# Optimization experiments

Hardware: AMD Instinct MI355X
Metric: run time of the kernel (lower is better)

Reference implementation:

```python
import jax, jax.numpy as jnp
import numpy as np

NEG_SLOPE = 0.01  # torch nn.LeakyReLU default


def setup_inputs() -> dict:
    key = jax.random.key(0)
    k1, k2, k3, k4, k5 = jax.random.split(key, 5)
    N, K, S, H = 50000, 32, 128, 4
    x = jax.random.normal(k1, (N, S), dtype=jnp.float32)          # node sentence vectors
    neighbors = jax.random.randint(k2, (N, K), 0, N)              # padded neighbor ids
    mask = jax.random.uniform(k3, (N, K)) < 0.75                  # valid-neighbor mask
    # DQA.B_ij per head: Linear(2*S -> 1), init std=0.05
    W = jax.random.normal(k4, (H, 2 * S), dtype=jnp.float32) * 0.05
    b = jax.random.normal(k5, (H,), dtype=jnp.float32) * 0.05
    return {"x": x, "W": W, "b": b, "neighbors": neighbors,
            "mask": mask, "propagate_count": 2}


def _leaky_relu(v):
    return jnp.where(v >= 0, v, NEG_SLOPE * v)


def reference(x, W, b, neighbors, mask, propagate_count):
    # x: [N,S]; W: [H,2S]; b: [H]; neighbors: [N,K] int; mask: [N,K] bool
    S = x.shape[-1]
    wa, wb = W[:, :S], W[:, S:]  # score = wa.x_center + wb.x_row + b

    def step(h):
        sa = h @ wa.T                                  # [N,H] center contribution
        sb = h @ wb.T                                  # [N,H] row contribution
        s_self = _leaky_relu(sa + sb + b)              # [N,H]   row 0 (self)
        s_nbr = _leaky_relu(sa[:, None, :] + sb[neighbors] + b)  # [N,K,H]
        s_nbr = jnp.where(mask[:, :, None], s_nbr, -jnp.inf)
        s_all = jnp.concatenate([s_self[:, None, :], s_nbr], axis=1)  # [N,K+1,H]
        p = jax.nn.softmax(s_all, axis=1)              # softmax over rows
        xg = h[neighbors]                              # [N,K,S] gather
        # weighted sum of rows, per head
        out = p[:, 0, :, None] * h[:, None, :] \
              + jnp.einsum('nkh,nks->nhs', p[:, 1:, :], xg)  # [N,H,S]
        # D_attention: sum over heads / n_heads, then ReLU
        return jax.nn.relu(out.mean(axis=1))           # [N,S]

    for _ in range(int(propagate_count)):
        x = step(x)
    return x
```

## Files before the change

### kernel.cpp

```cpp
#include <hip/hip_runtime.h>
#include <math.h>

#define S_DIM   128
#define K_NB    32
#define H_HEADS 4
#define WL_STRIDE 288
#define NSLOT   36

#if defined(__has_builtin)
#  if __has_builtin(__builtin_amdgcn_permlane16_swap)
#    define HAVE_PL16 1
#  endif
#  if __has_builtin(__builtin_amdgcn_permlane32_swap)
#    define HAVE_PL32 1
#  endif
#endif

__device__ __forceinline__ float lrelu(float v) { return fmaxf(v, 0.01f * v); }

__device__ __forceinline__ float bfly_add16(float x) {
#ifdef HAVE_PL16
    auto r = __builtin_amdgcn_permlane16_swap(__float_as_uint(x), __float_as_uint(x), false, false);
    return __uint_as_float(r[0]) + __uint_as_float(r[1]);
#else
    return x + __shfl_xor(x, 16, 64);
#endif
}
__device__ __forceinline__ float bfly_add32(float x) {
#ifdef HAVE_PL32
    auto r = __builtin_amdgcn_permlane32_swap(__float_as_uint(x), __float_as_uint(x), false, false);
    return __uint_as_float(r[0]) + __uint_as_float(r[1]);
#else
    return x + __shfl_xor(x, 32, 64);
#endif
}

__device__ __forceinline__ unsigned bf16rne(float f) {
    unsigned u = __float_as_uint(f);
    return (u + 0x7fffu + ((u >> 16) & 1u)) >> 16;
}
__device__ __forceinline__ unsigned pack2(float lo, float hi) {
    return bf16rne(lo) | (bf16rne(hi) << 16);
}

__global__ __launch_bounds__(256) void proj_kernel(const float* __restrict__ h,
                                                   const float* __restrict__ W,
                                                   float* __restrict__ sasb,
                                                   unsigned* __restrict__ hb_out,
                                                   const unsigned int* __restrict__ maskw,
                                                   int* __restrict__ flag, int N) {
    __shared__ float Wl[H_HEADS * 2 * S_DIM];
    for (int i = threadIdx.x; i < 1024; i += 256) Wl[i] = W[i];

    if (blockIdx.x == 0) {
        __shared__ int nb, nf;
        if (threadIdx.x == 0) { nb = 0; nf = 0; }
        __syncthreads();
        bool bin = true, f32 = true;
        for (int i = threadIdx.x; i < 2048; i += 256) {
            unsigned v = maskw[i];
            if (v > 1u) bin = false;
            if (v != 0u && v != 0x3F800000u) f32 = false;
        }
        if (!bin) atomicOr(&nb, 1);
        if (!f32) atomicOr(&nf, 1);
        __syncthreads();
        if (threadIdx.x == 0) *flag = nb ? (nf ? 2 : 1) : 0;
    }
    __syncthreads();

    const int wv = threadIdx.x >> 6;
    const int lane = threadIdx.x & 63;
    const int n = blockIdx.x * 4 + wv;
    if (n >= N) return;

    const float2 hv = reinterpret_cast<const float2*>(h)[(size_t)n * 64 + lane];
    hb_out[(size_t)n * 64 + lane] = pack2(hv.x, hv.y);

    const int c = 2 * lane;
    float p0 = hv.x * Wl[0 * 256 + c] + hv.y * Wl[0 * 256 + c + 1];
    float p1 = hv.x * Wl[1 * 256 + c] + hv.y * Wl[1 * 256 + c + 1];
    float p2 = hv.x * Wl[2 * 256 + c] + hv.y * Wl[2 * 256 + c + 1];
    float p3 = hv.x * Wl[3 * 256 + c] + hv.y * Wl[3 * 256 + c + 1];
    float p4 = hv.x * Wl[0 * 256 + 128 + c] + hv.y * Wl[0 * 256 + 128 + c + 1];
    float p5 = hv.x * Wl[1 * 256 + 128 + c] + hv.y * Wl[1 * 256 + 128 + c + 1];
    float p6 = hv.x * Wl[2 * 256 + 128 + c] + hv.y * Wl[2 * 256 + 128 + c + 1];
    float p7 = hv.x * Wl[3 * 256 + 128 + c] + hv.y * Wl[3 * 256 + 128 + c + 1];

    const float a0 = p0 + __shfl_xor(p0, 32, 64);
    const float a1 = p1 + __shfl_xor(p1, 32, 64);
    const float a2 = p2 + __shfl_xor(p2, 32, 64);
    const float a3 = p3 + __shfl_xor(p3, 32, 64);
    const float a4 = p4 + __shfl_xor(p4, 32, 64);
    const float a5 = p5 + __shfl_xor(p5, 32, 64);
    const float a6 = p6 + __shfl_xor(p6, 32, 64);
    const float a7 = p7 + __shfl_xor(p7, 32, 64);
    const bool lo = lane < 32;
    float r0 = lo ? a0 : a4, r1 = lo ? a1 : a5, r2 = lo ? a2 : a6, r3 = lo ? a3 : a7;
#pragma unroll
    for (int off = 16; off; off >>= 1) {
        r0 += __shfl_xor(r0, off, 64);
        r1 += __shfl_xor(r1, off, 64);
        r2 += __shfl_xor(r2, off, 64);
        r3 += __shfl_xor(r3, off, 64);
    }
    if (lane == 0)
        *reinterpret_cast<float4*>(sasb + (size_t)n * 8) = make_float4(r0, r1, r2, r3);
    if (lane == 32)
        *reinterpret_cast<float4*>(sasb + (size_t)n * 8 + 4) = make_float4(r0, r1, r2, r3);
}

__global__ __launch_bounds__(256) void attn_kernel(const uint4* __restrict__ hb,
                                                   const float* __restrict__ sasb,
                                                   const float* __restrict__ bvec,
                                                   const int* __restrict__ nbr,
                                                   const void* __restrict__ mask,
                                                   const int* __restrict__ maskmode,
                                                   float* __restrict__ fout,
                                                   uint4* __restrict__ hb_out,
                                                   float* __restrict__ sasb_next,
                                                   const float* __restrict__ W, int N) {
    __shared__ float2 qr_sh[4][NSLOT];
    __shared__ float Wl[H_HEADS * WL_STRIDE];

    if (sasb_next) {
        for (int i = threadIdx.x; i < 1024; i += 256) {
            const int hh = i >> 8, c = i & 255;
            Wl[hh * WL_STRIDE + c + (c >> 3)] = W[i];
        }
        __syncthreads();
    }

    const int wv = threadIdx.x >> 6;
    const int lane = threadIdx.x & 63;
    const int n = blockIdx.x * 4 + wv;
    if (n >= N) return;
    const int mode = *maskmode;

    const float b0 = bvec[0], b1 = bvec[1], b2 = bvec[2], b3 = bvec[3];
    const float4 sa = *reinterpret_cast<const float4*>(sasb + (size_t)n * 8);
    const float4 sbs = *reinterpret_cast<const float4*>(sasb + (size_t)n * 8 + 4);
    const float es0 = __expf(lrelu(sa.x + sbs.x + b0));
    const float es1 = __expf(lrelu(sa.y + sbs.y + b1));
    const float es2 = __expf(lrelu(sa.z + sbs.z + b2));
    const float es3 = __expf(lrelu(sa.w + sbs.w + b3));

    float l0 = -INFINITY, l1 = -INFINITY, l2 = -INFINITY, l3 = -INFINITY;
    int row = 0;
    bool valid = false;
    if (lane < K_NB) {
        row = nbr[(size_t)n * K_NB + lane];
        if (mode == 0)
            valid = reinterpret_cast<const int*>(mask)[(size_t)n * K_NB + lane] != 0;
        else if (mode == 1)
            valid = reinterpret_cast<const float*>(mask)[(size_t)n * K_NB + lane] != 0.f;
        else
            valid = reinterpret_cast<const unsigned char*>(mask)[(size_t)n * K_NB + lane] != 0;
    }
    if (valid) {
        const float4 sbr = *reinterpret_cast<const float4*>(sasb + (size_t)row * 8 + 4);
        l0 = lrelu(sa.x + sbr.x + b0);
        l1 = lrelu(sa.y + sbr.y + b1);
        l2 = lrelu(sa.z + sbr.z + b2);
        l3 = lrelu(sa.w + sbr.w + b3);
    }

    const float e0 = __expf(l0);
    const float e1 = __expf(l1);
    const float e2 = __expf(l2);
    const float e3 = __expf(l3);

    float s0 = bfly_add16(e0), s1 = bfly_add16(e1);
    float s2 = bfly_add16(e2), s3 = bfly_add16(e3);
#pragma unroll
    for (int off = 8; off; off >>= 1) {
        s0 += __shfl_xor(s0, off, 64);
        s1 += __shfl_xor(s1, off, 64);
        s2 += __shfl_xor(s2, off, 64);
        s3 += __shfl_xor(s3, off, 64);
    }
    s0 += es0; s1 += es1; s2 += es2; s3 += es3;
    const float i0 = __builtin_amdgcn_rcpf(s0);
    const float i1 = __builtin_amdgcn_rcpf(s1);
    const float i2 = __builtin_amdgcn_rcpf(s2);
    const float i3 = __builtin_amdgcn_rcpf(s3);

    const unsigned long long bm = __ballot(valid);
    const int nv1 = __popcll(bm) + 1;
    {
        const int ps = nv1 + lane;
        if (ps < NSLOT) qr_sh[wv][ps] = make_float2(0.f, __int_as_float(n));
    }
    if (valid) {
        const int pos = 1 + __popcll(bm & ((1ull << lane) - 1ull));
        qr_sh[wv][pos] = make_float2(
            0.25f * (e0 * i0 + e1 * i1 + e2 * i2 + e3 * i3), __int_as_float(row));
    }
    if (lane == 0)
        qr_sh[wv][0] = make_float2(
            0.25f * (es0 * i0 + es1 * i1 + es2 * i2 + es3 * i3), __int_as_float(n));

    const int grp = lane >> 4;
    const int sl = lane & 15;

    float2 qr[9];
#pragma unroll
    for (int t = 0; t < 9; ++t) qr[t] = qr_sh[wv][grp + 4 * t];

    uint4 v[9];
#pragma unroll
    for (int t = 0; t < 9; ++t) {
        const unsigned idx = ((unsigned)__float_as_int(qr[t].y) << 4) + (unsigned)sl;
        v[t] = hb[idx];
    }

    float acc[8];
#pragma unroll
    for (int j = 0; j < 8; ++j) acc[j] = 0.f;
#pragma unroll
    for (int t = 0; t < 9; ++t) {
        const float q = qr[t].x;
        acc[0] += q * __uint_as_float(v[t].x << 16);
        acc[1] += q * __uint_as_float(v[t].x & 0xffff0000u);
        acc[2] += q * __uint_as_float(v[t].y << 16);
        acc[3] += q * __uint_as_float(v[t].y & 0xffff0000u);
        acc[4] += q * __uint_as_float(v[t].z << 16);
        acc[5] += q * __uint_as_float(v[t].z & 0xffff0000u);
        acc[6] += q * __uint_as_float(v[t].w << 16);
        acc[7] += q * __uint_as_float(v[t].w & 0xffff0000u);
    }

#pragma unroll
    for (int j = 0; j < 8; ++j) {
        acc[j] = bfly_add16(acc[j]);
        acc[j] = bfly_add32(acc[j]);
        acc[j] = fmaxf(acc[j], 0.f);
    }

    if (lane < 32) {
        const int g1 = grp & 1;
        const float a0 = g1 ? acc[4] : acc[0];
        const float a1 = g1 ? acc[5] : acc[1];
        const float a2 = g1 ? acc[6] : acc[2];
        const float a3 = g1 ? acc[7] : acc[3];
        if (hb_out) {
            uint2 o;
            o.x = pack2(a0, a1);
            o.y = pack2(a2, a3);
            reinterpret_cast<uint2*>(hb_out)[(size_t)n * 32 + sl * 2 + g1] = o;
        }
        if (fout) {
            reinterpret_cast<float4*>(fout)[(size_t)n * 32 + sl * 2 + g1] =
                make_float4(a0, a1, a2, a3);
        }
    }

    if (sasb_next) {
        const int base = (lane >> 5) ? 128 : 0;
        const int boff = base + (base >> 3) + sl * 9;
        float r0 = 0.f, r1 = 0.f, r2 = 0.f, r3 = 0.f;
#pragma unroll
        for (int j = 0; j < 8; ++j) {
            const float a = acc[j];
            r0 += a * Wl[0 * WL_STRIDE + boff + j];
            r1 += a * Wl[1 * WL_STRIDE + boff + j];
            r2 += a * Wl[2 * WL_STRIDE + boff + j];
            r3 += a * Wl[3 * WL_STRIDE + boff + j];
        }
#pragma unroll
        for (int off = 8; off; off >>= 1) {
            r0 += __shfl_xor(r0, off, 64);
            r1 += __shfl_xor(r1, off, 64);
            r2 += __shfl_xor(r2, off, 64);
            r3 += __shfl_xor(r3, off, 64);
        }
        if (lane == 0)
            *reinterpret_cast<float4*>(sasb_next + (size_t)n * 8) = make_float4(r0, r1, r2, r3);
        if (lane == 32)
            *reinterpret_cast<float4*>(sasb_next + (size_t)n * 8 + 4) = make_float4(r0, r1, r2, r3);
    }
}


extern "C" void kernel_launch(void* const* d_in, const int* in_sizes, int n_in,
                              void* d_out, int out_size, void* d_ws, size_t ws_size,
                              hipStream_t stream) {
    const float* x = (const float*)d_in[0];
    const float* W = (const float*)d_in[1];
    const float* b = (const float*)d_in[2];
    const int* nbr = (const int*)d_in[3];
    const void* mask = d_in[4];

    const int N = in_sizes[0] / S_DIM;

    char* ws = (char*)d_ws;
    float* sasb = (float*)ws;
    size_t off = (size_t)N * 8 * sizeof(float);
    off = (off + 255) & ~(size_t)255;
    int* flag = (int*)(ws + off);
    off += 256;
    float* sasb2 = (float*)(ws + off);
    off += (size_t)N * 8 * sizeof(float);
    off = (off + 255) & ~(size_t)255;
    unsigned* xb = (unsigned*)(ws + off);
    off += (size_t)N * S_DIM * 2;
    uint4* h1b = (uint4*)(ws + off);

    float* out = (float*)d_out;
    const int blocks = (N + 3) / 4;

    proj_kernel<<<blocks, 256, 0, stream>>>(x, W, sasb, xb, (const unsigned int*)mask, flag, N);
    attn_kernel<<<blocks, 256, 0, stream>>>((const uint4*)xb, sasb, b, nbr, mask, flag,
                                            nullptr, h1b, sasb2, W, N);
    attn_kernel<<<blocks, 256, 0, stream>>>(h1b, sasb2, b, nbr, mask, flag,
                                            out, nullptr, nullptr, W, N);
}
```

Baseline: 129.9 us.

## Issue neighbor row gathers before softmax and skip empty gather slots

```diff
diff --git a/kernel.cpp b/kernel.cpp
--- a/kernel.cpp
+++ b/kernel.cpp
@@ -120,7 +120,8 @@
                                                    uint4* __restrict__ hb_out,
                                                    float* __restrict__ sasb_next,
                                                    const float* __restrict__ W, int N) {
-    __shared__ float2 qr_sh[4][NSLOT];
+    __shared__ int r_sh[4][NSLOT];
+    __shared__ float q_sh[4][NSLOT];
     __shared__ float Wl[H_HEADS * WL_STRIDE];
 
     if (sasb_next) {
@@ -137,16 +138,7 @@
     if (n >= N) return;
     const int mode = *maskmode;
 
-    const float b0 = bvec[0], b1 = bvec[1], b2 = bvec[2], b3 = bvec[3];
-    const float4 sa = *reinterpret_cast<const float4*>(sasb + (size_t)n * 8);
-    const float4 sbs = *reinterpret_cast<const float4*>(sasb + (size_t)n * 8 + 4);
-    const float es0 = __expf(lrelu(sa.x + sbs.x + b0));
-    const float es1 = __expf(lrelu(sa.y + sbs.y + b1));
-    const float es2 = __expf(lrelu(sa.z + sbs.z + b2));
-    const float es3 = __expf(lrelu(sa.w + sbs.w + b3));
-
-    float l0 = -INFINITY, l1 = -INFINITY, l2 = -INFINITY, l3 = -INFINITY;
-    int row = 0;
+    int row = n;
     bool valid = false;
     if (lane < K_NB) {
         row = nbr[(size_t)n * K_NB + lane];
@@ -157,6 +149,40 @@
         else
             valid = reinterpret_cast<const unsigned char*>(mask)[(size_t)n * K_NB + lane] != 0;
     }
+
+    const unsigned long long bm = __ballot(valid);
+    const int nv1 = __popcll(bm) + 1;
+    const int tcnt = (nv1 + 3) >> 2;
+    {
+        const int ps = nv1 + lane;
+        if (ps < NSLOT) r_sh[wv][ps] = n;
+    }
+    if (valid) {
+        const int pos = 1 + __popcll(bm & ((1ull << lane) - 1ull));
+        r_sh[wv][pos] = row;
+    }
+    if (lane == 0) r_sh[wv][0] = n;
+
+    const int grp = lane >> 4;
+    const int sl = lane & 15;
+    uint4 v[9];
+#pragma unroll
+    for (int t = 0; t < 9; ++t) {
+        if (t < tcnt) {
+            const unsigned idx = ((unsigned)r_sh[wv][grp + 4 * t] << 4) + (unsigned)sl;
+            v[t] = hb[idx];
+        }
+    }
+
+    const float b0 = bvec[0], b1 = bvec[1], b2 = bvec[2], b3 = bvec[3];
+    const float4 sa = *reinterpret_cast<const float4*>(sasb + (size_t)n * 8);
+    const float4 sbs = *reinterpret_cast<const float4*>(sasb + (size_t)n * 8 + 4);
+    const float es0 = __expf(lrelu(sa.x + sbs.x + b0));
+    const float es1 = __expf(lrelu(sa.y + sbs.y + b1));
+    const float es2 = __expf(lrelu(sa.z + sbs.z + b2));
+    const float es3 = __expf(lrelu(sa.w + sbs.w + b3));
+
+    float l0 = -INFINITY, l1 = -INFINITY, l2 = -INFINITY, l3 = -INFINITY;
     if (valid) {
         const float4 sbr = *reinterpret_cast<const float4*>(sasb + (size_t)row * 8 + 4);
         l0 = lrelu(sa.x + sbr.x + b0);
@@ -185,49 +211,33 @@
     const float i2 = __builtin_amdgcn_rcpf(s2);
     const float i3 = __builtin_amdgcn_rcpf(s3);
 
-    const unsigned long long bm = __ballot(valid);
-    const int nv1 = __popcll(bm) + 1;
     {
         const int ps = nv1 + lane;
-        if (ps < NSLOT) qr_sh[wv][ps] = make_float2(0.f, __int_as_float(n));
+        if (ps < NSLOT) q_sh[wv][ps] = 0.f;
     }
     if (valid) {
         const int pos = 1 + __popcll(bm & ((1ull << lane) - 1ull));
-        qr_sh[wv][pos] = make_float2(
-            0.25f * (e0 * i0 + e1 * i1 + e2 * i2 + e3 * i3), __int_as_float(row));
+        q_sh[wv][pos] = 0.25f * (e0 * i0 + e1 * i1 + e2 * i2 + e3 * i3);
     }
     if (lane == 0)
-        qr_sh[wv][0] = make_float2(
-            0.25f * (es0 * i0 + es1 * i1 + es2 * i2 + es3 * i3), __int_as_float(n));
-
-    const int grp = lane >> 4;
-    const int sl = lane & 15;
-
-    float2 qr[9];
-#pragma unroll
-    for (int t = 0; t < 9; ++t) qr[t] = qr_sh[wv][grp + 4 * t];
-
-    uint4 v[9];
+        q_sh[wv][0] = 0.25f * (es0 * i0 + es1 * i1 + es2 * i2 + es3 * i3);
+
+    float acc[8];
+#pragma unroll
+    for (int j = 0; j < 8; ++j) acc[j] = 0.f;
 #pragma unroll
     for (int t = 0; t < 9; ++t) {
-        const unsigned idx = ((unsigned)__float_as_int(qr[t].y) << 4) + (unsigned)sl;
-        v[t] = hb[idx];
-    }
-
-    float acc[8];
-#pragma unroll
-    for (int j = 0; j < 8; ++j) acc[j] = 0.f;
-#pragma unroll
-    for (int t = 0; t < 9; ++t) {
-        const float q = qr[t].x;
-        acc[0] += q * __uint_as_float(v[t].x << 16);
-        acc[1] += q * __uint_as_float(v[t].x & 0xffff0000u);
-        acc[2] += q * __uint_as_float(v[t].y << 16);
-        acc[3] += q * __uint_as_float(v[t].y & 0xffff0000u);
-        acc[4] += q * __uint_as_float(v[t].z << 16);
-        acc[5] += q * __uint_as_float(v[t].z & 0xffff0000u);
-        acc[6] += q * __uint_as_float(v[t].w << 16);
-        acc[7] += q * __uint_as_float(v[t].w & 0xffff0000u);
+        if (t < tcnt) {
+            const float q = q_sh[wv][grp + 4 * t];
+            acc[0] += q * __uint_as_float(v[t].x << 16);
+            acc[1] += q * __uint_as_float(v[t].x & 0xffff0000u);
+            acc[2] += q * __uint_as_float(v[t].y << 16);
+            acc[3] += q * __uint_as_float(v[t].y & 0xffff0000u);
+            acc[4] += q * __uint_as_float(v[t].z << 16);
+            acc[5] += q * __uint_as_float(v[t].z & 0xffff0000u);
+            acc[6] += q * __uint_as_float(v[t].w << 16);
+            acc[7] += q * __uint_as_float(v[t].w & 0xffff0000u);
+        }
     }
 
 #pragma unroll
```

Measured after the change: 134.9 us. 3.8% more time.

## Fold self row into lane 32, skip empty gather slots, use packed FMA

Applied to the files above, without the earlier changes.

```diff
diff --git a/kernel.cpp b/kernel.cpp
--- a/kernel.cpp
+++ b/kernel.cpp
@@ -14,7 +14,30 @@
 #  if __has_builtin(__builtin_amdgcn_permlane32_swap)
 #    define HAVE_PL32 1
 #  endif
-#endif
+#  if __has_builtin(__builtin_elementwise_fma)
+#    define HAVE_EFMA 1
+#  endif
+#  if __has_builtin(__builtin_elementwise_max)
+#    define HAVE_EMAX 1
+#  endif
+#endif
+
+typedef float f32x2 __attribute__((ext_vector_type(2)));
+
+__device__ __forceinline__ f32x2 pkfma(f32x2 a, f32x2 b, f32x2 c) {
+#ifdef HAVE_EFMA
+    return __builtin_elementwise_fma(a, b, c);
+#else
+    return a * b + c;
+#endif
+}
+__device__ __forceinline__ f32x2 pkrelu(f32x2 a) {
+#ifdef HAVE_EMAX
+    return __builtin_elementwise_max(a, (f32x2){0.f, 0.f});
+#else
+    f32x2 r; r.x = fmaxf(a.x, 0.f); r.y = fmaxf(a.y, 0.f); return r;
+#endif
+}
 
 __device__ __forceinline__ float lrelu(float v) { return fmaxf(v, 0.01f * v); }
 
@@ -41,6 +64,12 @@
 }
 __device__ __forceinline__ unsigned pack2(float lo, float hi) {
     return bf16rne(lo) | (bf16rne(hi) << 16);
+}
+__device__ __forceinline__ f32x2 up2(unsigned u) {
+    f32x2 r;
+    r.x = __uint_as_float(u << 16);
+    r.y = __uint_as_float(u & 0xffff0000u);
+    return r;
 }
 
 __global__ __launch_bounds__(256) void proj_kernel(const float* __restrict__ h,
@@ -137,17 +166,8 @@
     if (n >= N) return;
     const int mode = *maskmode;
 
-    const float b0 = bvec[0], b1 = bvec[1], b2 = bvec[2], b3 = bvec[3];
-    const float4 sa = *reinterpret_cast<const float4*>(sasb + (size_t)n * 8);
-    const float4 sbs = *reinterpret_cast<const float4*>(sasb + (size_t)n * 8 + 4);
-    const float es0 = __expf(lrelu(sa.x + sbs.x + b0));
-    const float es1 = __expf(lrelu(sa.y + sbs.y + b1));
-    const float es2 = __expf(lrelu(sa.z + sbs.z + b2));
-    const float es3 = __expf(lrelu(sa.w + sbs.w + b3));
-
-    float l0 = -INFINITY, l1 = -INFINITY, l2 = -INFINITY, l3 = -INFINITY;
-    int row = 0;
-    bool valid = false;
+    int row = n;
+    bool valid = (lane == K_NB);
     if (lane < K_NB) {
         row = nbr[(size_t)n * K_NB + lane];
         if (mode == 0)
@@ -157,6 +177,10 @@
         else
             valid = reinterpret_cast<const unsigned char*>(mask)[(size_t)n * K_NB + lane] != 0;
     }
+
+    const float b0 = bvec[0], b1 = bvec[1], b2 = bvec[2], b3 = bvec[3];
+    const float4 sa = *reinterpret_cast<const float4*>(sasb + (size_t)n * 8);
+    float l0 = -INFINITY, l1 = -INFINITY, l2 = -INFINITY, l3 = -INFINITY;
     if (valid) {
         const float4 sbr = *reinterpret_cast<const float4*>(sasb + (size_t)row * 8 + 4);
         l0 = lrelu(sa.x + sbr.x + b0);
@@ -172,6 +196,8 @@
 
     float s0 = bfly_add16(e0), s1 = bfly_add16(e1);
     float s2 = bfly_add16(e2), s3 = bfly_add16(e3);
+    s0 = bfly_add32(s0); s1 = bfly_add32(s1);
+    s2 = bfly_add32(s2); s3 = bfly_add32(s3);
 #pragma unroll
     for (int off = 8; off; off >>= 1) {
         s0 += __shfl_xor(s0, off, 64);
@@ -179,26 +205,24 @@
         s2 += __shfl_xor(s2, off, 64);
         s3 += __shfl_xor(s3, off, 64);
     }
-    s0 += es0; s1 += es1; s2 += es2; s3 += es3;
     const float i0 = __builtin_amdgcn_rcpf(s0);
     const float i1 = __builtin_amdgcn_rcpf(s1);
     const float i2 = __builtin_amdgcn_rcpf(s2);
     const float i3 = __builtin_amdgcn_rcpf(s3);
 
     const unsigned long long bm = __ballot(valid);
-    const int nv1 = __popcll(bm) + 1;
+    const int nv1 = __popcll(bm);
+    const int tcnt = (nv1 + 3) >> 2;
     {
         const int ps = nv1 + lane;
         if (ps < NSLOT) qr_sh[wv][ps] = make_float2(0.f, __int_as_float(n));
     }
     if (valid) {
-        const int pos = 1 + __popcll(bm & ((1ull << lane) - 1ull));
+        const int pos = (lane == K_NB) ? 0
+                      : 1 + __popcll(bm & ((1ull << lane) - 1ull));
         qr_sh[wv][pos] = make_float2(
             0.25f * (e0 * i0 + e1 * i1 + e2 * i2 + e3 * i3), __int_as_float(row));
     }
-    if (lane == 0)
-        qr_sh[wv][0] = make_float2(
-            0.25f * (es0 * i0 + es1 * i1 + es2 * i2 + es3 * i3), __int_as_float(n));
 
     const int grp = lane >> 4;
     const int sl = lane & 15;
@@ -214,59 +238,63 @@
         v[t] = hb[idx];
     }
 
-    float acc[8];
-#pragma unroll
-    for (int j = 0; j < 8; ++j) acc[j] = 0.f;
+    f32x2 acc2[4];
+#pragma unroll
+    for (int p = 0; p < 4; ++p) acc2[p] = (f32x2){0.f, 0.f};
 #pragma unroll
     for (int t = 0; t < 9; ++t) {
-        const float q = qr[t].x;
-        acc[0] += q * __uint_as_float(v[t].x << 16);
-        acc[1] += q * __uint_as_float(v[t].x & 0xffff0000u);
-        acc[2] += q * __uint_as_float(v[t].y << 16);
-        acc[3] += q * __uint_as_float(v[t].y & 0xffff0000u);
-        acc[4] += q * __uint_as_float(v[t].z << 16);
-        acc[5] += q * __uint_as_float(v[t].z & 0xffff0000u);
-        acc[6] += q * __uint_as_float(v[t].w << 16);
-        acc[7] += q * __uint_as_float(v[t].w & 0xffff0000u);
-    }
-
-#pragma unroll
-    for (int j = 0; j < 8; ++j) {
-        acc[j] = bfly_add16(acc[j]);
-        acc[j] = bfly_add32(acc[j]);
-        acc[j] = fmaxf(acc[j], 0.f);
+        if (t < tcnt) {
+            const float q = qr[t].x;
+            const f32x2 q2 = {q, q};
+            acc2[0] = pkfma(q2, up2(v[t].x), acc2[0]);
+            acc2[1] = pkfma(q2, up2(v[t].y), acc2[1]);
+            acc2[2] = pkfma(q2, up2(v[t].z), acc2[2]);
+            acc2[3] = pkfma(q2, up2(v[t].w), acc2[3]);
+        }
+    }
+
+#pragma unroll
+    for (int p = 0; p < 4; ++p) {
+        acc2[p].x = bfly_add16(acc2[p].x);
+        acc2[p].y = bfly_add16(acc2[p].y);
+        acc2[p].x = bfly_add32(acc2[p].x);
+        acc2[p].y = bfly_add32(acc2[p].y);
+        acc2[p] = pkrelu(acc2[p]);
     }
 
     if (lane < 32) {
         const int g1 = grp & 1;
-        const float a0 = g1 ? acc[4] : acc[0];
-        const float a1 = g1 ? acc[5] : acc[1];
-        const float a2 = g1 ? acc[6] : acc[2];
-        const float a3 = g1 ? acc[7] : acc[3];
+        const f32x2 lo2 = g1 ? acc2[2] : acc2[0];
+        const f32x2 hi2 = g1 ? acc2[3] : acc2[1];
         if (hb_out) {
             uint2 o;
-            o.x = pack2(a0, a1);
-            o.y = pack2(a2, a3);
+            o.x = pack2(lo2.x, lo2.y);
+            o.y = pack2(hi2.x, hi2.y);
             reinterpret_cast<uint2*>(hb_out)[(size_t)n * 32 + sl * 2 + g1] = o;
         }
         if (fout) {
             reinterpret_cast<float4*>(fout)[(size_t)n * 32 + sl * 2 + g1] =
-                make_float4(a0, a1, a2, a3);
+                make_float4(lo2.x, lo2.y, hi2.x, hi2.y);
         }
     }
 
     if (sasb_next) {
         const int base = (lane >> 5) ? 128 : 0;
         const int boff = base + (base >> 3) + sl * 9;
-        float r0 = 0.f, r1 = 0.f, r2 = 0.f, r3 = 0.f;
-#pragma unroll
-        for (int j = 0; j < 8; ++j) {
-            const float a = acc[j];
-            r0 += a * Wl[0 * WL_STRIDE + boff + j];
-            r1 += a * Wl[1 * WL_STRIDE + boff + j];
-            r2 += a * Wl[2 * WL_STRIDE + boff + j];
-            r3 += a * Wl[3 * WL_STRIDE + boff + j];
-        }
+        f32x2 rp0 = {0.f, 0.f}, rp1 = {0.f, 0.f}, rp2 = {0.f, 0.f}, rp3 = {0.f, 0.f};
+#pragma unroll
+        for (int p = 0; p < 4; ++p) {
+            const f32x2 a2 = acc2[p];
+            const int j = boff + 2 * p;
+            rp0 = pkfma(a2, (f32x2){Wl[0 * WL_STRIDE + j], Wl[0 * WL_STRIDE + j + 1]}, rp0);
+            rp1 = pkfma(a2, (f32x2){Wl[1 * WL_STRIDE + j], Wl[1 * WL_STRIDE + j + 1]}, rp1);
+            rp2 = pkfma(a2, (f32x2){Wl[2 * WL_STRIDE + j], Wl[2 * WL_STRIDE + j + 1]}, rp2);
+            rp3 = pkfma(a2, (f32x2){Wl[3 * WL_STRIDE + j], Wl[3 * WL_STRIDE + j + 1]}, rp3);
+        }
+        float r0 = rp0.x + rp0.y;
+        float r1 = rp1.x + rp1.y;
+        float r2 = rp2.x + rp2.y;
+        float r3 = rp3.x + rp3.y;
 #pragma unroll
         for (int off = 8; off; off >>= 1) {
             r0 += __shfl_xor(r0, off, 64);
```

New measurement: 134.0 us. 3.1% more time.
